# Performance work log

Hardware: AMD Instinct MI355X
Metric: run time of the kernel (lower is better)

Reference implementation:

```python
import jax, jax.numpy as jnp
import numpy as np

BN_EPS = 1e-5


def setup_inputs() -> dict:
    key = jax.random.key(0)
    ks = jax.random.split(key, 12)
    B, C, N = 8, 256, 2048
    s = 1.0 / np.sqrt(C)
    x = jax.random.normal(ks[0], (B, C, N), dtype=jnp.float32)
    gamma = jnp.ones((C,), jnp.float32)
    beta = jnp.zeros((C,), jnp.float32)
    Wq = jax.random.normal(ks[1], (C, C), jnp.float32) * s
    bq = jnp.zeros((C,), jnp.float32)
    Wk = jax.random.normal(ks[2], (C, C), jnp.float32) * s
    bk = jnp.zeros((C,), jnp.float32)
    Wv = jax.random.normal(ks[3], (C, C), jnp.float32) * s
    bv = jnp.zeros((C,), jnp.float32)
    Wp = jax.random.normal(ks[4], (C, C), jnp.float32) * s
    bp = jnp.zeros((C,), jnp.float32)
    return {"x": x, "gamma": gamma, "beta": beta, "Wq": Wq, "bq": bq,
            "Wk": Wk, "bk": bk, "Wv": Wv, "bv": bv, "Wp": Wp, "bp": bp}


def reference(x, gamma, beta, Wq, bq, Wk, bk, Wv, bv, Wp, bp):
    B, C, N = x.shape
    # BatchNorm1d (training-mode batch stats): normalize per channel over (B, N)
    mean = jnp.mean(x, axis=(0, 2), keepdims=True)            # [1,C,1]
    var = jnp.mean(jnp.square(x - mean), axis=(0, 2), keepdims=True)
    h = (x - mean) * jax.lax.rsqrt(var + BN_EPS)
    h = h * gamma[None, :, None] + beta[None, :, None]
    # 1x1 Conv1d projections == per-position channel GEMMs
    q = jnp.einsum('oc,bcn->bno', Wq, h) + bq[None, None, :]  # [B,N,C]
    k = jnp.einsum('oc,bcn->bon', Wk, h) + bk[None, :, None]  # [B,C,N]
    v = jnp.einsum('oc,bcn->bno', Wv, h) + bv[None, None, :]  # [B,N,C]
    scale = jnp.asarray(C, x.dtype) ** -0.5
    w = jnp.einsum('bnc,bcm->bnm', q, k) * scale              # [B,N,N]
    w = jax.nn.softmax(w, axis=-1)
    h = jnp.einsum('bnm,bmc->bnc', w, v)                      # [B,N,C]
    out = jnp.einsum('oc,bnc->bon', Wp, h) + bp[None, :, None]  # [B,C,N]
    return x + out
```

## Files before the change

### kernel.cpp

```cpp
#include <hip/hip_runtime.h>
#include <hip/hip_fp16.h>

typedef _Float16 f16x8 __attribute__((ext_vector_type(8)));
typedef _Float16 f16x4 __attribute__((ext_vector_type(4)));
typedef float f32x4 __attribute__((ext_vector_type(4)));
typedef float f32x16 __attribute__((ext_vector_type(16)));

#define MFMA16(a, b, c) __builtin_amdgcn_mfma_f32_16x16x32_f16(a, b, c, 0, 0, 0)
#define MFMA32(a, b, c) __builtin_amdgcn_mfma_f32_32x32x16_f16(a, b, c, 0, 0, 0)

__device__ __forceinline__ void gload_lds16(const _Float16* g, void* l) {
    __builtin_amdgcn_global_load_lds(
        (const __attribute__((address_space(1))) void*)g,
        (__attribute__((address_space(3))) void*)l, 16, 0, 0);
}

__device__ __forceinline__ unsigned pkh(float a, float b) {
    typedef __fp16 fp16v2 __attribute__((ext_vector_type(2)));
    fp16v2 h = __builtin_amdgcn_cvt_pkrtz(a, b);
    return __builtin_bit_cast(unsigned, h);
}

__device__ __forceinline__ float fexp2(float x) {
#if __has_builtin(__builtin_amdgcn_exp2f)
    return __builtin_amdgcn_exp2f(x);
#else
    return exp2f(x);
#endif
}

__global__ __launch_bounds__(256) void trans_stats_kernel(
    const float* __restrict__ x, _Float16* __restrict__ xt,
    float* __restrict__ sums)
{
    __shared__ float tile[64][65];
    int t = threadIdx.x;
    int b = blockIdx.z, c0 = blockIdx.y * 64, n0 = blockIdx.x * 64;
    int nl = t & 63, cq = t >> 6;
#pragma unroll
    for (int r = 0; r < 16; ++r) {
        int cl = cq * 16 + r;
        tile[cl][nl] = x[((size_t)b * 256 + c0 + cl) * 2048 + n0 + nl];
    }
    __syncthreads();
    int cl2 = t & 63, nq = t >> 6;
#pragma unroll
    for (int r = 0; r < 16; ++r) {
        int nl2 = nq * 16 + r;
        xt[((size_t)b * 2048 + n0 + nl2) * 256 + c0 + cl2] = (_Float16)tile[cl2][nl2];
    }
    if (t < 64) {
        float s = 0.f, ss = 0.f;
#pragma unroll
        for (int j = 0; j < 64; ++j) {
            float v = tile[t][j];
            s += v; ss += v * v;
        }
        atomicAdd(&sums[c0 + t], s);
        atomicAdd(&sums[256 + c0 + t], ss);
    }
}

__global__ __launch_bounds__(256) void fold_kernel(
    const float* __restrict__ Wq, const float* __restrict__ Wk,
    const float* __restrict__ Wv, const float* __restrict__ Wp,
    const float* __restrict__ bq, const float* __restrict__ bk,
    const float* __restrict__ bv,
    const float* __restrict__ gamma, const float* __restrict__ beta,
    const float* __restrict__ sums,
    _Float16* __restrict__ wbf, float* __restrict__ bfold)
{
    int t = threadIdx.x, bid = blockIdx.x;
    if (bid >= 192) {
        int i = (bid - 192) * 256 + t;
        wbf[3 * 65536 + i] = (_Float16)Wp[i];
        return;
    }
    __shared__ float sc[256], sh[256];
    if (t < 256) {
        float mean = sums[t] * (1.f / 16384.f);
        float var  = sums[256 + t] * (1.f / 16384.f) - mean * mean;
        float rstd = rsqrtf(var + 1e-5f);
        float s = rstd * gamma[t];
        sc[t] = s;
        sh[t] = beta[t] - mean * s;
    }
    __syncthreads();
    const float QS = 0.09016844005556021f;
    int mat = bid >> 6;
    int o = (bid & 63) * 4 + (t >> 6);
    int lane = t & 63;
    const float* W  = (mat == 0) ? Wq : (mat == 1) ? Wk : Wv;
    const float* bb = (mat == 0) ? bq : (mat == 1) ? bk : bv;
    float qs = (mat == 0) ? QS : 1.f;
    int wslot = (mat == 0) ? 0 : (mat == 1) ? 131072 : 65536;
    float dot = 0.f;
    _Float16* wd = wbf + wslot + o * 256;
#pragma unroll
    for (int i = 0; i < 4; ++i) {
        int c = lane * 4 + i;
        float wv_ = W[o * 256 + c];
        dot += wv_ * sh[c];
        wd[c] = (_Float16)(wv_ * sc[c] * qs);
    }
#pragma unroll
    for (int off = 32; off > 0; off >>= 1) dot += __shfl_down(dot, off, 64);
    if (lane == 0) bfold[mat * 256 + o] = qs * (bb[o] + dot);
}

template<int BN, int WGM, int WGN, typename OT, bool BIAS_I, bool RES, int EPI>
__global__ __launch_bounds__(256, 3) void gemm_nt(
    const _Float16* __restrict__ Aall, long strideA,
    const _Float16* __restrict__ Ball, long strideB,
    const float* __restrict__ bias,
    const float* __restrict__ resid, long strideR,
    OT* __restrict__ Call, long strideC, int Nn,
    OT* __restrict__ Cauxall)
{
    constexpr int BM = 128;
    constexpr int WR = BM / WGM;
    constexpr int WC = BN / WGN;
    constexpr int FM = WR / 16, FN = WC / 16;
    constexpr int BUFSZ = 8192 + BN * 64;
    constexpr int NI = 8 + BN / 16;
    constexpr int PW = NI / 4;

    int b = blockIdx.z;
    const _Float16* A  = Aall + (size_t)b * strideA;
    const _Float16* Bm = Ball + (size_t)b * strideB;
    OT* C = Call + (size_t)b * strideC;
    int i0 = blockIdx.y * BM, j0 = blockIdx.x * BN;

    __shared__ __align__(16) char lds[2 * BUFSZ];

    int t = threadIdx.x, lane = t & 63, w = t >> 6;
    int lr = lane & 15, lg = lane >> 4;
    int wm = w % WGM, wn = w / WGM;

    int soff = (lane >> 2) * 256 + (((lane & 3) ^ ((lane >> 3) & 3))) * 8;
    int lgx16 = ((lg ^ ((lr >> 1) & 3))) * 16;

    f32x4 acc[FM][FN] = {};

    auto stage = [&](int kk, int buf) {
#pragma unroll
        for (int i = 0; i < PW; ++i) {
            int u = w * PW + i;
            if (u < 8)
                gload_lds16(A + (size_t)(i0 + u * 16) * 256 + kk * 32 + soff,
                            lds + buf * BUFSZ + u * 1024);
            else
                gload_lds16(Bm + (size_t)(j0 + (u - 8) * 16) * 256 + kk * 32 + soff,
                            lds + buf * BUFSZ + 8192 + (u - 8) * 1024);
        }
    };

    stage(0, 0);
    __syncthreads();
    int buf = 0;
#pragma unroll
    for (int kk = 0; kk < 8; ++kk) {
        if (kk + 1 < 8) stage(kk + 1, buf ^ 1);
        const char* ab = lds + buf * BUFSZ;
        const char* bb = ab + 8192;
        f16x8 af[FM], bf[FN];
#pragma unroll
        for (int f = 0; f < FM; ++f)
            af[f] = *(const f16x8*)(ab + (wm * WR + f * 16 + lr) * 64 + lgx16);
#pragma unroll
        for (int f = 0; f < FN; ++f)
            bf[f] = *(const f16x8*)(bb + (wn * WC + f * 16 + lr) * 64 + lgx16);
        __builtin_amdgcn_s_setprio(1);
#pragma unroll
        for (int fm = 0; fm < FM; ++fm)
#pragma unroll
            for (int fn = 0; fn < FN; ++fn)
                acc[fm][fn] = MFMA16(af[fm], bf[fn], acc[fm][fn]);
        __builtin_amdgcn_s_setprio(0);
        __syncthreads();
        buf ^= 1;
    }
    if constexpr (EPI == 0) {
#pragma unroll
        for (int fm = 0; fm < FM; ++fm)
#pragma unroll
            for (int fn = 0; fn < FN; ++fn)
#pragma unroll
                for (int rr = 0; rr < 4; ++rr) {
                    int row = i0 + wm * WR + fm * 16 + lg * 4 + rr;
                    int col = j0 + wn * WC + fn * 16 + lr;
                    float vv = acc[fm][fn][rr] + (BIAS_I ? bias[row] : bias[col]);
                    if (RES) vv += resid[(size_t)b * strideR + (size_t)row * Nn + col];
                    C[(size_t)row * Nn + col] = (OT)vv;
                }
    } else if constexpr (EPI == 1) {
#pragma unroll
        for (int fm = 0; fm < FM; ++fm)
#pragma unroll
            for (int fn = 0; fn < FN; ++fn) {
                int row0 = i0 + wm * WR + fm * 16 + lg * 4;
                int col  = j0 + wn * WC + fn * 16 + lr;
                f16x4 q4;
#pragma unroll
                for (int rr = 0; rr < 4; ++rr)
                    q4[rr] = (_Float16)(acc[fm][fn][rr] + bias[row0 + rr]);
                int mt = col >> 5, mloc = col & 31;
                int ks = row0 >> 4;
                int ln2 = mloc + 32 * (lg >> 1);
                size_t off = (((size_t)mt * 16 + ks) * 64 + ln2) * 8 + (lg & 1) * 4;
                *(f16x4*)((_Float16*)C + off) = q4;
            }
    } else {
        bool vreg = (EPI == 2) || (j0 >= 256);
#pragma unroll
        for (int fm = 0; fm < FM; ++fm)
#pragma unroll
            for (int fn = 0; fn < FN; ++fn) {
                int row0 = i0 + wm * WR + fm * 16 + lg * 4;
                int col  = j0 + wn * WC + fn * 16 + lr;
                if (vreg) {
                    int colv = (EPI == 3) ? col - 256 : col;
                    const float bv_ = (EPI == 3) ? bias[256 + col] : bias[colv];
                    f16x4 q4;
#pragma unroll
                    for (int rr = 0; rr < 4; ++rr)
                        q4[rr] = (_Float16)(acc[fm][fn][rr] + bv_);
                    int mt = row0 >> 5, ms = (row0 >> 4) & 1;
                    int dt = colv >> 5, dloc = colv & 31;
                    int ln2 = dloc + 32 * (lg >> 1);
                    size_t off = ((((size_t)mt * 2 + ms) * 8 + dt) * 64 + ln2) * 8 + (lg & 1) * 4;
                    OT* dst = (EPI == 3) ? (Cauxall + (size_t)b * strideC) : C;
                    *(f16x4*)((_Float16*)dst + off) = q4;
                } else {
#pragma unroll
                    for (int rr = 0; rr < 4; ++rr) {
                        float vv = acc[fm][fn][rr] + bias[col];
                        C[(size_t)(row0 + rr) * 256 + col] = (OT)vv;
                    }
                }
            }
    }
}

__global__ __launch_bounds__(256, 2) void attn9_kernel(
    const _Float16* __restrict__ qb, const _Float16* __restrict__ kfrag,
    const _Float16* __restrict__ vfrag,
    _Float16* __restrict__ Opart, float* __restrict__ lpart,
    int nsp, int mspan)
{
    int id = blockIdx.x;
    int b = id & 7;
    int rest = id >> 3;
    int qblk = rest & 15, sp = rest >> 4;
    int T = mspan >> 5;

    __shared__ __align__(16) char lds[81920];

    int t = threadIdx.x, ln = t & 63, w = t >> 6;
    int col = ln & 31, hi = ln >> 5;

    const _Float16* kg = kfrag + (size_t)b * 524288 + (size_t)(sp * T) * 8192 + ln * 8;
    const _Float16* vg = vfrag + (size_t)b * 524288 + (size_t)(sp * T) * 8192 + ln * 8;
    int c0 = w * 4;
    int frd = ln * 16;

    f16x8 qf[16];
    {
        const _Float16* qp = qb + ((size_t)b * 2048 + qblk * 128 + w * 32 + col) * 256 + hi * 8;
#pragma unroll
        for (int ks = 0; ks < 16; ++ks) qf[ks] = *(const f16x8*)(qp + ks * 16);
    }

    f32x16 oacc[8] = {};
    float l_run = 0.f;
    unsigned W[8];

#pragma unroll
    for (int i = 0; i < 4; ++i) {
        int c = c0 + i;
        gload_lds16(kg + c * 512,        lds + c * 1024);
        gload_lds16(kg + 8192 + c * 512, lds + 16384 + c * 1024);
        gload_lds16(vg + c * 512,        lds + 32768 + c * 1024);
        gload_lds16(vg + 8192 + c * 512, lds + 49152 + c * 1024);
    }
    asm volatile("s_waitcnt vmcnt(0)" ::: "memory");
    __builtin_amdgcn_sched_barrier(0);
    __builtin_amdgcn_s_barrier();
    {
        f32x16 sn = {};
        __builtin_amdgcn_s_setprio(1);
#pragma unroll
        for (int ks = 0; ks < 16; ++ks) {
            f16x8 kf = *(const f16x8*)(lds + ks * 1024 + frd);
            sn = MFMA32(kf, qf[ks], sn);
        }
        __builtin_amdgcn_s_setprio(0);
        float pv_[16];
#pragma unroll
        for (int i = 0; i < 16; ++i) pv_[i] = fexp2(sn[i] - 16.f);
        float psum = ((pv_[0]+pv_[1]) + (pv_[2]+pv_[3])) + ((pv_[4]+pv_[5]) + (pv_[6]+pv_[7]))
                   + ((pv_[8]+pv_[9]) + (pv_[10]+pv_[11])) + ((pv_[12]+pv_[13]) + (pv_[14]+pv_[15]));
        psum += __shfl_xor(psum, 32, 64);
        l_run = psum;
        W[0] = pkh(pv_[0],  pv_[1]);  W[1] = pkh(pv_[2],  pv_[3]);
        W[2] = pkh(pv_[4],  pv_[5]);  W[3] = pkh(pv_[6],  pv_[7]);
        W[4] = pkh(pv_[8],  pv_[9]);  W[5] = pkh(pv_[10], pv_[11]);
        W[6] = pkh(pv_[12], pv_[13]); W[7] = pkh(pv_[14], pv_[15]);
    }
    __builtin_amdgcn_s_barrier();

    for (int tt = 0; tt < T - 1; ++tt) {
        const char* kb = lds + ((tt + 1) & 1) * 16384;
        const char* vb = lds + 32768 + (tt % 3) * 16384;
        if (tt + 2 < T) {
            const _Float16* sK = kg + (size_t)(tt + 2) * 8192;
            const _Float16* sV = vg + (size_t)(tt + 2) * 8192;
            char* kd = lds + (tt & 1) * 16384;
            char* vd = lds + 32768 + ((tt + 2) % 3) * 16384;
#pragma unroll
            for (int i = 0; i < 4; ++i) {
                gload_lds16(sK + (c0 + i) * 512, kd + (c0 + i) * 1024);
                gload_lds16(sV + (c0 + i) * 512, vd + (c0 + i) * 1024);
            }
        }
        union { unsigned u[4]; f16x8 v; } pf0, pf1;
        {
            unsigned sx0 = hi ? W[0] : W[2], sx1 = hi ? W[1] : W[3];
            unsigned r0 = __shfl_xor(sx0, 32, 64), r1 = __shfl_xor(sx1, 32, 64);
            pf0.u[0] = hi ? r0 : W[0]; pf0.u[1] = hi ? r1 : W[1];
            pf0.u[2] = hi ? W[2] : r0; pf0.u[3] = hi ? W[3] : r1;
        }
        {
            unsigned sx0 = hi ? W[4] : W[6], sx1 = hi ? W[5] : W[7];
            unsigned r0 = __shfl_xor(sx0, 32, 64), r1 = __shfl_xor(sx1, 32, 64);
            pf1.u[0] = hi ? r0 : W[4]; pf1.u[1] = hi ? r1 : W[5];
            pf1.u[2] = hi ? W[6] : r0; pf1.u[3] = hi ? W[7] : r1;
        }
        f32x16 sn = {};
        __builtin_amdgcn_s_setprio(1);
#pragma unroll
        for (int g = 0; g < 4; ++g) {
#pragma unroll
            for (int k2 = 0; k2 < 4; ++k2) {
                int ks = g * 4 + k2;
                f16x8 kf = *(const f16x8*)(kb + ks * 1024 + frd);
                sn = MFMA32(kf, qf[ks], sn);
            }
#pragma unroll
            for (int k2 = 0; k2 < 4; ++k2) {
                int idx = g * 4 + k2;
                f16x8 vf = *(const f16x8*)(vb + 16384 * 0 + idx * 1024 + frd);
                oacc[idx & 7] = MFMA32(vf, (g < 2) ? pf0.v : pf1.v, oacc[idx & 7]);
            }
        }
        __builtin_amdgcn_s_setprio(0);
        {
            float pv_[16];
#pragma unroll
            for (int i = 0; i < 16; ++i) pv_[i] = fexp2(sn[i] - 16.f);
            float psum = ((pv_[0]+pv_[1]) + (pv_[2]+pv_[3])) + ((pv_[4]+pv_[5]) + (pv_[6]+pv_[7]))
                       + ((pv_[8]+pv_[9]) + (pv_[10]+pv_[11])) + ((pv_[12]+pv_[13]) + (pv_[14]+pv_[15]));
            psum += __shfl_xor(psum, 32, 64);
            l_run += psum;
            W[0] = pkh(pv_[0],  pv_[1]);  W[1] = pkh(pv_[2],  pv_[3]);
            W[2] = pkh(pv_[4],  pv_[5]);  W[3] = pkh(pv_[6],  pv_[7]);
            W[4] = pkh(pv_[8],  pv_[9]);  W[5] = pkh(pv_[10], pv_[11]);
            W[6] = pkh(pv_[12], pv_[13]); W[7] = pkh(pv_[14], pv_[15]);
        }
        asm volatile("s_waitcnt vmcnt(4)" ::: "memory");
        __builtin_amdgcn_sched_barrier(0);
        __builtin_amdgcn_s_barrier();
    }

    asm volatile("s_waitcnt vmcnt(0)" ::: "memory");
    __builtin_amdgcn_sched_barrier(0);
    __builtin_amdgcn_s_barrier();
    {
        const char* vb = lds + 32768 + ((T - 1) % 3) * 16384;
        union { unsigned u[4]; f16x8 v; } pf0, pf1;
        {
            unsigned sx0 = hi ? W[0] : W[2], sx1 = hi ? W[1] : W[3];
            unsigned r0 = __shfl_xor(sx0, 32, 64), r1 = __shfl_xor(sx1, 32, 64);
            pf0.u[0] = hi ? r0 : W[0]; pf0.u[1] = hi ? r1 : W[1];
            pf0.u[2] = hi ? W[2] : r0; pf0.u[3] = hi ? W[3] : r1;
        }
        {
            unsigned sx0 = hi ? W[4] : W[6], sx1 = hi ? W[5] : W[7];
            unsigned r0 = __shfl_xor(sx0, 32, 64), r1 = __shfl_xor(sx1, 32, 64);
            pf1.u[0] = hi ? r0 : W[4]; pf1.u[1] = hi ? r1 : W[5];
            pf1.u[2] = hi ? W[6] : r0; pf1.u[3] = hi ? W[7] : r1;
        }
        __builtin_amdgcn_s_setprio(1);
#pragma unroll
        for (int idx = 0; idx < 16; ++idx) {
            f16x8 vf = *(const f16x8*)(vb + idx * 1024 + frd);
            oacc[idx & 7] = MFMA32(vf, (idx < 8) ? pf0.v : pf1.v, oacc[idx & 7]);
        }
        __builtin_amdgcn_s_setprio(0);
    }
    __builtin_amdgcn_s_barrier();

    _Float16* tr = (_Float16*)(lds + w * 16640);
    float invl = 1.0f / l_run;
#pragma unroll
    for (int dt = 0; dt < 8; ++dt)
#pragma unroll
        for (int g = 0; g < 4; ++g) {
            f16x4 q4;
#pragma unroll
            for (int e = 0; e < 4; ++e) q4[e] = (_Float16)(oacc[dt][g * 4 + e] * invl);
            int d0 = dt * 32 + g * 8 + 4 * hi;
            *(f16x4*)(tr + col * 260 + d0) = q4;
        }
    size_t region = ((size_t)((sp * 8 + b) * 16 + qblk)) * 32768;
    int rrow = ln >> 1, h = ln & 1;
    const _Float16* srcr = tr + rrow * 260 + h * 128;
    _Float16* dstr = Opart + region + (size_t)(w * 32 + rrow) * 256 + h * 128;
#pragma unroll
    for (int i = 0; i < 16; ++i)
        *(f16x8*)(dstr + i * 8) = *(const f16x8*)(srcr + i * 8);

    if (hi == 0) {
        int qi = w * 32 + col;
        lpart[((sp * 8 + b) * 16 + qblk) * 128 + qi] = l_run;
    }
}

__global__ __launch_bounds__(256) void combine3_kernel(
    const _Float16* __restrict__ Opart, const float* __restrict__ lpart,
    _Float16* __restrict__ abuf, int nsp)
{
    int id = blockIdx.x;
    int b = id & 7, qb = (id >> 3) & 15, dh = id >> 7;
    int t = threadIdx.x;
    __shared__ float cf[4][128];
    if (t < 128) {
        float l[4], s = 0.f;
        for (int sp = 0; sp < nsp; ++sp) {
            l[sp] = lpart[((sp * 8 + b) * 16 + qb) * 128 + t];
            s += l[sp];
        }
        float inv = 1.0f / s;
        for (int sp = 0; sp < nsp; ++sp) cf[sp][t] = l[sp] * inv;
    }
    __syncthreads();
    size_t rb = ((size_t)(b * 16 + qb)) * 32768;
#pragma unroll
    for (int i = 0; i < 8; ++i) {
        int flat = i * 2048 + t * 8;
        int qi = flat >> 7, dl = flat & 127;
        float acc[8] = {};
        for (int sp = 0; sp < nsp; ++sp) {
            f16x8 v = *(const f16x8*)(Opart + (size_t)sp * 4194304 + rb +
                                      (size_t)qi * 256 + dh * 128 + dl);
            float c = cf[sp][qi];
#pragma unroll
            for (int e = 0; e < 8; ++e) acc[e] += c * (float)v[e];
        }
        f16x8 r;
#pragma unroll
        for (int e = 0; e < 8; ++e) r[e] = (_Float16)acc[e];
        *(f16x8*)(abuf + ((size_t)b * 2048 + qb * 128 + qi) * 256 + dh * 128 + dl) = r;
    }
}

extern "C" void kernel_launch(void* const* d_in, const int* in_sizes, int n_in,
                              void* d_out, int out_size, void* d_ws, size_t ws_size,
                              hipStream_t stream) {
    const float* x     = (const float*)d_in[0];
    const float* gamma = (const float*)d_in[1];
    const float* beta  = (const float*)d_in[2];
    const float* Wq    = (const float*)d_in[3];
    const float* bq    = (const float*)d_in[4];
    const float* Wk    = (const float*)d_in[5];
    const float* bk    = (const float*)d_in[6];
    const float* Wv    = (const float*)d_in[7];
    const float* bv    = (const float*)d_in[8];
    const float* Wp    = (const float*)d_in[9];
    const float* bp    = (const float*)d_in[10];
    float* out = (float*)d_out;

    char* ws = (char*)d_ws;
    float* sums  = (float*)ws;
    float* bfold = (float*)(ws + 2048);
    float* lpart = (float*)(ws + 8192);
    _Float16* wbf   = (_Float16*)(ws + 524288);
    _Float16* xt    = (_Float16*)(ws + 1048576);
    _Float16* qbuf  = (_Float16*)(ws + 9437184);
    _Float16* kfrag = (_Float16*)(ws + 17825792);
    _Float16* vfrag = (_Float16*)(ws + 26214400);
    _Float16* Opart = (_Float16*)(ws + 34603008);
    _Float16* abuf  = xt;

    int nsp = (ws_size >= (size_t)34603008 + 4ull * 8388608ull) ? 4 : 2;
    int mspan = 2048 / nsp;

    const long SB = 524288;

    hipMemsetAsync(sums, 0, 2048, stream);
    trans_stats_kernel<<<dim3(32, 4, 8), 256, 0, stream>>>(x, xt, sums);
    fold_kernel<<<448, 256, 0, stream>>>(Wq, Wk, Wv, Wp, bq, bk, bv,
                                         gamma, beta, sums, wbf, bfold);
    gemm_nt<128, 2, 2, _Float16, false, false, 3><<<dim3(4, 16, 8), 256, 0, stream>>>(
        xt, SB, wbf, 0, bfold, nullptr, 0, qbuf, SB, 256, vfrag);
    gemm_nt<64, 4, 1, _Float16, true, false, 1><<<dim3(32, 2, 8), 256, 0, stream>>>(
        wbf + 131072, 0, xt, SB, bfold + 256, nullptr, 0, kfrag, SB, 2048, (_Float16*)nullptr);
    attn9_kernel<<<128 * nsp, 256, 0, stream>>>(qbuf, kfrag, vfrag, Opart, lpart,
                                                nsp, mspan);
    combine3_kernel<<<256, 256, 0, stream>>>(Opart, lpart, abuf, nsp);
    gemm_nt<64, 4, 1, float, true, true, 0><<<dim3(32, 2, 8), 256, 0, stream>>>(
        wbf + 196608, 0, abuf, SB, bp, x, SB, out, SB, 2048, (float*)nullptr);
}
```

Before: 108.2 us.

## Restructure attention to 8-wave blocks splitting head dim and streaming Q from global

Measured after the change: 180.1 us. +66.4%, slower.

```diff
diff --git a/kernel.cpp b/kernel.cpp
--- a/kernel.cpp
+++ b/kernel.cpp
@@ -93,9 +93,8 @@
     const float* W  = (mat == 0) ? Wq : (mat == 1) ? Wk : Wv;
     const float* bb = (mat == 0) ? bq : (mat == 1) ? bk : bv;
     float qs = (mat == 0) ? QS : 1.f;
-    int wslot = (mat == 0) ? 0 : (mat == 1) ? 131072 : 65536;
     float dot = 0.f;
-    _Float16* wd = wbf + wslot + o * 256;
+    _Float16* wd = wbf + mat * 65536 + o * 256;
 #pragma unroll
     for (int i = 0; i < 4; ++i) {
         int c = lane * 4 + i;
@@ -204,46 +203,38 @@
 #pragma unroll
                 for (int rr = 0; rr < 4; ++rr)
                     q4[rr] = (_Float16)(acc[fm][fn][rr] + bias[row0 + rr]);
+                bool isq = row0 < 256;
+                int ksr = isq ? row0 : (row0 - 256);
                 int mt = col >> 5, mloc = col & 31;
-                int ks = row0 >> 4;
+                int ks = ksr >> 4;
                 int ln2 = mloc + 32 * (lg >> 1);
                 size_t off = (((size_t)mt * 16 + ks) * 64 + ln2) * 8 + (lg & 1) * 4;
-                *(f16x4*)((_Float16*)C + off) = q4;
+                OT* dst = isq ? C : (Cauxall + (size_t)b * strideC);
+                *(f16x4*)((_Float16*)dst + off) = q4;
             }
     } else {
-        bool vreg = (EPI == 2) || (j0 >= 256);
 #pragma unroll
         for (int fm = 0; fm < FM; ++fm)
 #pragma unroll
             for (int fn = 0; fn < FN; ++fn) {
                 int row0 = i0 + wm * WR + fm * 16 + lg * 4;
                 int col  = j0 + wn * WC + fn * 16 + lr;
-                if (vreg) {
-                    int colv = (EPI == 3) ? col - 256 : col;
-                    const float bv_ = (EPI == 3) ? bias[256 + col] : bias[colv];
-                    f16x4 q4;
-#pragma unroll
-                    for (int rr = 0; rr < 4; ++rr)
-                        q4[rr] = (_Float16)(acc[fm][fn][rr] + bv_);
-                    int mt = row0 >> 5, ms = (row0 >> 4) & 1;
-                    int dt = colv >> 5, dloc = colv & 31;
-                    int ln2 = dloc + 32 * (lg >> 1);
-                    size_t off = ((((size_t)mt * 2 + ms) * 8 + dt) * 64 + ln2) * 8 + (lg & 1) * 4;
-                    OT* dst = (EPI == 3) ? (Cauxall + (size_t)b * strideC) : C;
-                    *(f16x4*)((_Float16*)dst + off) = q4;
-                } else {
-#pragma unroll
-                    for (int rr = 0; rr < 4; ++rr) {
-                        float vv = acc[fm][fn][rr] + bias[col];
-                        C[(size_t)(row0 + rr) * 256 + col] = (OT)vv;
-                    }
-                }
+                const float bv_ = bias[col];
+                f16x4 q4;
+#pragma unroll
+                for (int rr = 0; rr < 4; ++rr)
+                    q4[rr] = (_Float16)(acc[fm][fn][rr] + bv_);
+                int mt = row0 >> 5, ms = (row0 >> 4) & 1;
+                int dt = col >> 5, dloc = col & 31;
+                int ln2 = dloc + 32 * (lg >> 1);
+                size_t off = ((((size_t)mt * 2 + ms) * 8 + dt) * 64 + ln2) * 8 + (lg & 1) * 4;
+                *(f16x4*)((_Float16*)C + off) = q4;
             }
     }
 }
 
-__global__ __launch_bounds__(256, 2) void attn9_kernel(
-    const _Float16* __restrict__ qb, const _Float16* __restrict__ kfrag,
+__global__ __launch_bounds__(512, 4) void attn10_kernel(
+    const _Float16* __restrict__ qfrag, const _Float16* __restrict__ kfrag,
     const _Float16* __restrict__ vfrag,
     _Float16* __restrict__ Opart, float* __restrict__ lpart,
     int nsp, int mspan)
@@ -254,176 +245,118 @@
     int qblk = rest & 15, sp = rest >> 4;
     int T = mspan >> 5;
 
-    __shared__ __align__(16) char lds[81920];
+    __shared__ __align__(16) char lds[67584];
 
     int t = threadIdx.x, ln = t & 63, w = t >> 6;
+    int g = w & 3, h = w >> 2;
     int col = ln & 31, hi = ln >> 5;
 
     const _Float16* kg = kfrag + (size_t)b * 524288 + (size_t)(sp * T) * 8192 + ln * 8;
     const _Float16* vg = vfrag + (size_t)b * 524288 + (size_t)(sp * T) * 8192 + ln * 8;
-    int c0 = w * 4;
+    const _Float16* qg = qfrag + ((size_t)(b * 64 + qblk * 4 + g)) * 8192 + ln * 8;
+    int c0 = w * 2;
     int frd = ln * 16;
 
-    f16x8 qf[16];
-    {
-        const _Float16* qp = qb + ((size_t)b * 2048 + qblk * 128 + w * 32 + col) * 256 + hi * 8;
-#pragma unroll
-        for (int ks = 0; ks < 16; ++ks) qf[ks] = *(const f16x8*)(qp + ks * 16);
-    }
-
-    f32x16 oacc[8] = {};
+    f32x16 oacc[4] = {};
     float l_run = 0.f;
-    unsigned W[8];
-
-#pragma unroll
-    for (int i = 0; i < 4; ++i) {
-        int c = c0 + i;
-        gload_lds16(kg + c * 512,        lds + c * 1024);
-        gload_lds16(kg + 8192 + c * 512, lds + 16384 + c * 1024);
-        gload_lds16(vg + c * 512,        lds + 32768 + c * 1024);
-        gload_lds16(vg + 8192 + c * 512, lds + 49152 + c * 1024);
-    }
-    asm volatile("s_waitcnt vmcnt(0)" ::: "memory");
-    __builtin_amdgcn_sched_barrier(0);
-    __builtin_amdgcn_s_barrier();
-    {
+
+#pragma unroll
+    for (int i = 0; i < 2; ++i) {
+        gload_lds16(kg + (c0 + i) * 512, lds + (c0 + i) * 1024);
+        gload_lds16(vg + (c0 + i) * 512, lds + 32768 + (c0 + i) * 1024);
+    }
+    __syncthreads();
+
+    for (int tt = 0; tt < T; ++tt) {
+        int cur = tt & 1;
+        if (tt + 1 < T) {
+            const _Float16* sK = kg + (size_t)(tt + 1) * 8192;
+            const _Float16* sV = vg + (size_t)(tt + 1) * 8192;
+#pragma unroll
+            for (int i = 0; i < 2; ++i) {
+                gload_lds16(sK + (c0 + i) * 512, lds + (cur ^ 1) * 16384 + (c0 + i) * 1024);
+                gload_lds16(sV + (c0 + i) * 512, lds + 32768 + (cur ^ 1) * 16384 + (c0 + i) * 1024);
+            }
+        }
+        const char* kb = lds + cur * 16384;
+        const char* vb = lds + 32768 + cur * 16384;
+
         f32x16 sn = {};
+        f16x8 qv[4];
+#pragma unroll
+        for (int i = 0; i < 4; ++i) qv[i] = *(const f16x8*)(qg + i * 512);
         __builtin_amdgcn_s_setprio(1);
 #pragma unroll
         for (int ks = 0; ks < 16; ++ks) {
-            f16x8 kf = *(const f16x8*)(lds + ks * 1024 + frd);
-            sn = MFMA32(kf, qf[ks], sn);
+            f16x8 kf = *(const f16x8*)(kb + ks * 1024 + frd);
+            f16x8 qcur = qv[ks & 3];
+            if (ks + 4 < 16) qv[ks & 3] = *(const f16x8*)(qg + (ks + 4) * 512);
+            sn = MFMA32(kf, qcur, sn);
         }
         __builtin_amdgcn_s_setprio(0);
+
         float pv_[16];
 #pragma unroll
         for (int i = 0; i < 16; ++i) pv_[i] = fexp2(sn[i] - 16.f);
         float psum = ((pv_[0]+pv_[1]) + (pv_[2]+pv_[3])) + ((pv_[4]+pv_[5]) + (pv_[6]+pv_[7]))
                    + ((pv_[8]+pv_[9]) + (pv_[10]+pv_[11])) + ((pv_[12]+pv_[13]) + (pv_[14]+pv_[15]));
         psum += __shfl_xor(psum, 32, 64);
-        l_run = psum;
-        W[0] = pkh(pv_[0],  pv_[1]);  W[1] = pkh(pv_[2],  pv_[3]);
-        W[2] = pkh(pv_[4],  pv_[5]);  W[3] = pkh(pv_[6],  pv_[7]);
-        W[4] = pkh(pv_[8],  pv_[9]);  W[5] = pkh(pv_[10], pv_[11]);
-        W[6] = pkh(pv_[12], pv_[13]); W[7] = pkh(pv_[14], pv_[15]);
-    }
-    __builtin_amdgcn_s_barrier();
-
-    for (int tt = 0; tt < T - 1; ++tt) {
-        const char* kb = lds + ((tt + 1) & 1) * 16384;
-        const char* vb = lds + 32768 + (tt % 3) * 16384;
-        if (tt + 2 < T) {
-            const _Float16* sK = kg + (size_t)(tt + 2) * 8192;
-            const _Float16* sV = vg + (size_t)(tt + 2) * 8192;
-            char* kd = lds + (tt & 1) * 16384;
-            char* vd = lds + 32768 + ((tt + 2) % 3) * 16384;
-#pragma unroll
-            for (int i = 0; i < 4; ++i) {
-                gload_lds16(sK + (c0 + i) * 512, kd + (c0 + i) * 1024);
-                gload_lds16(sV + (c0 + i) * 512, vd + (c0 + i) * 1024);
-            }
-        }
+        l_run += psum;
+
+        unsigned W0[2], W1[2], W2[2], W3[2];
+        W0[0] = pkh(pv_[0],  pv_[1]);  W0[1] = pkh(pv_[2],  pv_[3]);
+        W1[0] = pkh(pv_[4],  pv_[5]);  W1[1] = pkh(pv_[6],  pv_[7]);
+        W2[0] = pkh(pv_[8],  pv_[9]);  W2[1] = pkh(pv_[10], pv_[11]);
+        W3[0] = pkh(pv_[12], pv_[13]); W3[1] = pkh(pv_[14], pv_[15]);
+
         union { unsigned u[4]; f16x8 v; } pf0, pf1;
         {
-            unsigned sx0 = hi ? W[0] : W[2], sx1 = hi ? W[1] : W[3];
+            unsigned sx0 = hi ? W0[0] : W1[0], sx1 = hi ? W0[1] : W1[1];
             unsigned r0 = __shfl_xor(sx0, 32, 64), r1 = __shfl_xor(sx1, 32, 64);
-            pf0.u[0] = hi ? r0 : W[0]; pf0.u[1] = hi ? r1 : W[1];
-            pf0.u[2] = hi ? W[2] : r0; pf0.u[3] = hi ? W[3] : r1;
+            pf0.u[0] = hi ? r0 : W0[0]; pf0.u[1] = hi ? r1 : W0[1];
+            pf0.u[2] = hi ? W1[0] : r0; pf0.u[3] = hi ? W1[1] : r1;
         }
         {
-            unsigned sx0 = hi ? W[4] : W[6], sx1 = hi ? W[5] : W[7];
+            unsigned sx0 = hi ? W2[0] : W3[0], sx1 = hi ? W2[1] : W3[1];
             unsigned r0 = __shfl_xor(sx0, 32, 64), r1 = __shfl_xor(sx1, 32, 64);
-            pf1.u[0] = hi ? r0 : W[4]; pf1.u[1] = hi ? r1 : W[5];
-            pf1.u[2] = hi ? W[6] : r0; pf1.u[3] = hi ? W[7] : r1;
-        }
-        f32x16 sn = {};
+            pf1.u[0] = hi ? r0 : W2[0]; pf1.u[1] = hi ? r1 : W2[1];
+            pf1.u[2] = hi ? W3[0] : r0; pf1.u[3] = hi ? W3[1] : r1;
+        }
+
         __builtin_amdgcn_s_setprio(1);
 #pragma unroll
-        for (int g = 0; g < 4; ++g) {
-#pragma unroll
-            for (int k2 = 0; k2 < 4; ++k2) {
-                int ks = g * 4 + k2;
-                f16x8 kf = *(const f16x8*)(kb + ks * 1024 + frd);
-                sn = MFMA32(kf, qf[ks], sn);
+        for (int ms = 0; ms < 2; ++ms)
+#pragma unroll
+            for (int j = 0; j < 4; ++j) {
+                f16x8 vf = *(const f16x8*)(vb + (ms * 8 + h * 4 + j) * 1024 + frd);
+                oacc[j] = MFMA32(vf, ms ? pf1.v : pf0.v, oacc[j]);
             }
-#pragma unroll
-            for (int k2 = 0; k2 < 4; ++k2) {
-                int idx = g * 4 + k2;
-                f16x8 vf = *(const f16x8*)(vb + 16384 * 0 + idx * 1024 + frd);
-                oacc[idx & 7] = MFMA32(vf, (g < 2) ? pf0.v : pf1.v, oacc[idx & 7]);
-            }
-        }
         __builtin_amdgcn_s_setprio(0);
-        {
-            float pv_[16];
-#pragma unroll
-            for (int i = 0; i < 16; ++i) pv_[i] = fexp2(sn[i] - 16.f);
-            float psum = ((pv_[0]+pv_[1]) + (pv_[2]+pv_[3])) + ((pv_[4]+pv_[5]) + (pv_[6]+pv_[7]))
-                       + ((pv_[8]+pv_[9]) + (pv_[10]+pv_[11])) + ((pv_[12]+pv_[13]) + (pv_[14]+pv_[15]));
-            psum += __shfl_xor(psum, 32, 64);
-            l_run += psum;
-            W[0] = pkh(pv_[0],  pv_[1]);  W[1] = pkh(pv_[2],  pv_[3]);
-            W[2] = pkh(pv_[4],  pv_[5]);  W[3] = pkh(pv_[6],  pv_[7]);
-            W[4] = pkh(pv_[8],  pv_[9]);  W[5] = pkh(pv_[10], pv_[11]);
-            W[6] = pkh(pv_[12], pv_[13]); W[7] = pkh(pv_[14], pv_[15]);
-        }
-        asm volatile("s_waitcnt vmcnt(4)" ::: "memory");
-        __builtin_amdgcn_sched_barrier(0);
-        __builtin_amdgcn_s_barrier();
-    }
-
-    asm volatile("s_waitcnt vmcnt(0)" ::: "memory");
-    __builtin_amdgcn_sched_barrier(0);
-    __builtin_amdgcn_s_barrier();
-    {
-        const char* vb = lds + 32768 + ((T - 1) % 3) * 16384;
-        union { unsigned u[4]; f16x8 v; } pf0, pf1;
-        {
-            unsigned sx0 = hi ? W[0] : W[2], sx1 = hi ? W[1] : W[3];
-            unsigned r0 = __shfl_xor(sx0, 32, 64), r1 = __shfl_xor(sx1, 32, 64);
-            pf0.u[0] = hi ? r0 : W[0]; pf0.u[1] = hi ? r1 : W[1];
-            pf0.u[2] = hi ? W[2] : r0; pf0.u[3] = hi ? W[3] : r1;
-        }
-        {
-            unsigned sx0 = hi ? W[4] : W[6], sx1 = hi ? W[5] : W[7];
-            unsigned r0 = __shfl_xor(sx0, 32, 64), r1 = __shfl_xor(sx1, 32, 64);
-            pf1.u[0] = hi ? r0 : W[4]; pf1.u[1] = hi ? r1 : W[5];
-            pf1.u[2] = hi ? W[6] : r0; pf1.u[3] = hi ? W[7] : r1;
-        }
-        __builtin_amdgcn_s_setprio(1);
-#pragma unroll
-        for (int idx = 0; idx < 16; ++idx) {
-            f16x8 vf = *(const f16x8*)(vb + idx * 1024 + frd);
-            oacc[idx & 7] = MFMA32(vf, (idx < 8) ? pf0.v : pf1.v, oacc[idx & 7]);
-        }
-        __builtin_amdgcn_s_setprio(0);
-    }
-    __builtin_amdgcn_s_barrier();
-
-    _Float16* tr = (_Float16*)(lds + w * 16640);
+
+        __syncthreads();
+    }
+
+    _Float16* tr = (_Float16*)(lds + w * 8448);
     float invl = 1.0f / l_run;
 #pragma unroll
-    for (int dt = 0; dt < 8; ++dt)
-#pragma unroll
-        for (int g = 0; g < 4; ++g) {
+    for (int j = 0; j < 4; ++j)
+#pragma unroll
+        for (int g4 = 0; g4 < 4; ++g4) {
             f16x4 q4;
 #pragma unroll
-            for (int e = 0; e < 4; ++e) q4[e] = (_Float16)(oacc[dt][g * 4 + e] * invl);
-            int d0 = dt * 32 + g * 8 + 4 * hi;
-            *(f16x4*)(tr + col * 260 + d0) = q4;
+            for (int e = 0; e < 4; ++e) q4[e] = (_Float16)(oacc[j][g4 * 4 + e] * invl);
+            *(f16x4*)(tr + col * 132 + j * 32 + g4 * 8 + 4 * hi) = q4;
         }
     size_t region = ((size_t)((sp * 8 + b) * 16 + qblk)) * 32768;
-    int rrow = ln >> 1, h = ln & 1;
-    const _Float16* srcr = tr + rrow * 260 + h * 128;
-    _Float16* dstr = Opart + region + (size_t)(w * 32 + rrow) * 256 + h * 128;
-#pragma unroll
-    for (int i = 0; i < 16; ++i)
+    int rrow = ln >> 1, hh = ln & 1;
+    const _Float16* srcr = tr + rrow * 132 + hh * 64;
+    _Float16* dstr = Opart + region + (size_t)(g * 32 + rrow) * 256 + h * 128 + hh * 64;
+#pragma unroll
+    for (int i = 0; i < 8; ++i)
         *(f16x8*)(dstr + i * 8) = *(const f16x8*)(srcr + i * 8);
 
-    if (hi == 0) {
-        int qi = w * 32 + col;
-        lpart[((sp * 8 + b) * 16 + qblk) * 128 + qi] = l_run;
-    }
+    if (h == 0 && hi == 0)
+        lpart[((sp * 8 + b) * 16 + qblk) * 128 + g * 32 + col] = l_run;
 }
 
 __global__ __launch_bounds__(256) void combine3_kernel(
@@ -486,7 +419,7 @@
     float* lpart = (float*)(ws + 8192);
     _Float16* wbf   = (_Float16*)(ws + 524288);
     _Float16* xt    = (_Float16*)(ws + 1048576);
-    _Float16* qbuf  = (_Float16*)(ws + 9437184);
+    _Float16* qfrag = (_Float16*)(ws + 9437184);
     _Float16* kfrag = (_Float16*)(ws + 17825792);
     _Float16* vfrag = (_Float16*)(ws + 26214400);
     _Float16* Opart = (_Float16*)(ws + 34603008);
@@ -501,12 +434,12 @@
     trans_stats_kernel<<<dim3(32, 4, 8), 256, 0, stream>>>(x, xt, sums);
     fold_kernel<<<448, 256, 0, stream>>>(Wq, Wk, Wv, Wp, bq, bk, bv,
                                          gamma, beta, sums, wbf, bfold);
-    gemm_nt<128, 2, 2, _Float16, false, false, 3><<<dim3(4, 16, 8), 256, 0, stream>>>(
-        xt, SB, wbf, 0, bfold, nullptr, 0, qbuf, SB, 256, vfrag);
-    gemm_nt<64, 4, 1, _Float16, true, false, 1><<<dim3(32, 2, 8), 256, 0, stream>>>(
-        wbf + 131072, 0, xt, SB, bfold + 256, nullptr, 0, kfrag, SB, 2048, (_Float16*)nullptr);
-    attn9_kernel<<<128 * nsp, 256, 0, stream>>>(qbuf, kfrag, vfrag, Opart, lpart,
-                                                nsp, mspan);
+    gemm_nt<64, 4, 1, _Float16, true, false, 1><<<dim3(32, 4, 8), 256, 0, stream>>>(
+        wbf, 0, xt, SB, bfold, nullptr, 0, qfrag, SB, 2048, kfrag);
+    gemm_nt<64, 4, 1, _Float16, false, false, 2><<<dim3(4, 16, 8), 256, 0, stream>>>(
+        xt, SB, wbf + 131072, 0, bfold + 512, nullptr, 0, vfrag, SB, 256, (_Float16*)nullptr);
+    attn10_kernel<<<128 * nsp, 512, 0, stream>>>(qfrag, kfrag, vfrag, Opart, lpart,
+                                                 nsp, mspan);
     combine3_kernel<<<256, 256, 0, stream>>>(Opart, lpart, abuf, nsp);
     gemm_nt<64, 4, 1, float, true, true, 0><<<dim3(32, 2, 8), 256, 0, stream>>>(
         wbf + 196608, 0, abuf, SB, bp, x, SB, out, SB, 2048, (float*)nullptr);
```
